# Kernel optimization log

Hardware: AMD Instinct MI355X
Metric: run time of the kernel (lower is better)

Reference implementation:

```python
import jax, jax.numpy as jnp
import numpy as np

NF = 24      # num_filters
KS = 5       # kernel_size
NB = 31      # num RBF basis
GAMMA = 0.1
EPS = 1e-3
B, H, W = 8, 180, 180


def setup_inputs() -> dict:
    key = jax.random.key(0)
    k1, k2, k3 = jax.random.split(key, 3)
    u = jax.random.uniform(k1, (B, 1, H, W), dtype=jnp.float32)
    f = jax.random.uniform(k2, (B, 1, H, W), dtype=jnp.float32)
    filters = jax.random.normal(k3, (NF, 1, KS, KS), dtype=jnp.float32) * 0.05
    mu = np.linspace(-1.0, 1.0, NB).astype(np.float32)
    x = np.linspace(-1.0, 1.0, 256).astype(np.float32)
    target = np.tanh(3.0 * x)
    basis = np.exp(-(x[:, None] - mu[None, :]) ** 2 / (2.0 * GAMMA ** 2))
    weights, _, _, _ = np.linalg.lstsq(basis, target, rcond=None)
    return {
        "u": u,
        "f": f,
        "filters": filters,
        "lambda_param": jnp.float32(0.1),
        "mu": jnp.asarray(mu),
        "weights": jnp.asarray(weights.astype(np.float32)),
    }


def reference(u, f, filters, lambda_param, mu, weights):
    dn = ("NCHW", "OIHW", "NCHW")
    pad = KS // 2
    # avg_pool2d(k=3, s=1, p=1) with count_include_pad=True (torch default): sum / 9
    u_sigma = jax.lax.reduce_window(
        u, 0.0, jax.lax.add,
        window_dimensions=(1, 1, 3, 3),
        window_strides=(1, 1, 1, 1),
        padding=[(0, 0), (0, 0), (1, 1), (1, 1)],
    ) / 9.0
    M = jnp.mean(u_sigma) + 0.001
    # all 24 per-filter convs as one grouped conv: [B,1,H,W] -> [B,NF,H,W]
    conv = jax.lax.conv_general_dilated(
        u, filters, (1, 1), [(pad, pad), (pad, pad)], dimension_numbers=dn
    )
    # RBF influence (identical frozen params for every filter)
    diff = conv[..., None] - mu                      # [B,NF,H,W,NB]
    phi = jnp.sum(weights * jnp.exp(-(diff ** 2) / (2.0 * GAMMA ** 2)), axis=-1)
    scaled_phi = (u_sigma / M) * phi                 # broadcast over NF channels
    # sum_i conv2d(scaled_phi_i, flip(k_i)) == one conv NF->1 with flipped kernels
    kT = jnp.flip(filters, axis=(2, 3)).transpose(1, 0, 2, 3)  # [1,NF,KS,KS]
    diffusion = jax.lax.conv_general_dilated(
        scaled_phi, kT, (1, 1), [(pad, pad), (pad, pad)], dimension_numbers=dn
    )
    reaction = lambda_param * (u - f) / (u * u + EPS)
    return jnp.clip(u - diffusion - reaction, 0.0, 1.0)
```

## Files before the change

### kernel.cpp

```cpp
#include <hip/hip_runtime.h>
#include <hip/hip_fp16.h>
#include <math.h>

#define HH 180
#define WW 180
#define BATCH 8
#define NF 24
#define NCP (NF / 2)
#define NB 31
#define HW (HH * WW)
#define NTOT (BATCH * HW)

#define TABN 1536
#define TAB_SCALE 512.0f
#define TAB_OFF 768.0f
#define L2E 1.4426950408889634f
#define RBF_L (-50.0f * L2E)

#if __has_builtin(__builtin_amdgcn_exp2f)
#define EXP2(x) __builtin_amdgcn_exp2f(x)
#else
#define EXP2(x) __expf((x) * 0.6931471805599453f)
#endif

typedef float v2f __attribute__((ext_vector_type(2)));

static __device__ __forceinline__ v2f splat2(float x) { v2f r; r.x = x; r.y = x; return r; }

__global__ __launch_bounds__(256) void k1_prepare(const float* __restrict__ u,
                                                  const float* __restrict__ wts,
                                                  const float* __restrict__ filters,
                                                  float* __restrict__ partials,
                                                  __half2* __restrict__ tab,
                                                  float* __restrict__ fT,
                                                  __half2* __restrict__ fTh) {
    __shared__ float sred[4];
    int blk = blockIdx.x, tid = threadIdx.x;
    if (blk < 128) {
        float v = 0.f;
        for (int i = blk * 256 + tid; i < NTOT / 4; i += 128 * 256) {
            float4 uv = ((const float4*)u)[i];
            int rem = (i * 4) % HW;
            int y = rem / WW, x0 = rem % WW;
            float cy = (y == 0 || y == HH - 1) ? 2.f : 3.f;
            float c0 = (x0 == 0) ? 2.f : 3.f;
            float c3 = (x0 + 3 == WW - 1) ? 2.f : 3.f;
            v += cy * (uv.x * c0 + (uv.y + uv.z) * 3.f + uv.w * c3);
        }
        #pragma unroll
        for (int off = 32; off; off >>= 1) v += __shfl_down(v, off, 64);
        int lane = tid & 63, wid = tid >> 6;
        if (lane == 0) sred[wid] = v;
        __syncthreads();
        if (tid == 0) partials[blk] = sred[0] + sred[1] + sred[2] + sred[3];
    } else if (blk < 134) {
        int e = (blk - 128) * 256 + tid;
        float w[NB];
        #pragma unroll
        for (int j = 0; j < NB; j++) w[j] = wts[j];
        float xa = -1.5f + (float)e * (1.f / TAB_SCALE);
        float xb = xa + (1.f / TAB_SCALE);
        float va = 0.f, vb = 0.f;
        #pragma unroll
        for (int j = 0; j < NB; j++) {
            float muj = -1.f + (float)j * (1.f / 15.f);
            float da = xa - muj, db = xb - muj;
            va = fmaf(w[j], EXP2(RBF_L * da * da), va);
            vb = fmaf(w[j], EXP2(RBF_L * db * db), vb);
        }
        tab[e] = __floats2half2_rn(va, vb - va);
    } else {
        for (int e = tid; e < NCP * 25; e += 256) {
            int cp = e / 25, k = e - cp * 25;
            float a = filters[(2 * cp) * 25 + k];
            float b = filters[(2 * cp + 1) * 25 + k];
            fT[2 * e] = a;
            fT[2 * e + 1] = b;
            fTh[e] = __floats2half2_rn(a, b);
        }
    }
}

#define TX 32
#define TY 12
#define TW 36
#define TH 16
#define TPTS (TW * TH)
#define UW 40
#define UH 20

static __device__ __forceinline__ float phi_lut(const __half2* stab, float c) {
    float tp = fmaf(c, TAB_SCALE, TAB_OFF);
    tp = fminf(fmaxf(tp, 0.f), (float)(TABN - 1));
    int i = (int)tp;
    float fr = tp - (float)i;
    float2 e = __half22float2(stab[i]);
    return fmaf(fr, e.y, e.x);
}

__global__ __launch_bounds__(256, 4) void k23_fused(const float* __restrict__ u,
                                                     const float* __restrict__ f,
                                                     const float* __restrict__ lam_p,
                                                     const float* __restrict__ partials,
                                                     const __half2* __restrict__ tab,
                                                     const v2f* __restrict__ fT2,
                                                     const __half2* __restrict__ fTh,
                                                     float* __restrict__ out) {
    __shared__ __align__(16) float su[UH * UW];
    __shared__ __align__(16) unsigned st[NCP * TPTS];
    __shared__ __align__(16) __half2 stab[TABN];
    __shared__ float sM[1];
    int b = blockIdx.z;
    int x0 = blockIdx.x * TX, y0 = blockIdx.y * TY;
    int tid = threadIdx.x;

    for (int e = tid; e < UH * UW; e += 256) {
        int r = e / UW, c = e - r * UW;
        int gy = y0 - 4 + r, gx = x0 - 4 + c;
        float v = 0.f;
        if (gy >= 0 && gy < HH && gx >= 0 && gx < WW) v = u[b * HW + gy * WW + gx];
        su[e] = v;
    }
    for (int e = tid; e < TABN / 4; e += 256)
        ((float4*)stab)[e] = ((const float4*)tab)[e];
    if (tid < 64) {
        float ps = partials[tid] + partials[tid + 64];
        #pragma unroll
        for (int off = 32; off; off >>= 1) ps += __shfl_down(ps, off, 64);
        if (tid == 0) sM[0] = 1.0f / (ps * (1.f / (9.f * (float)NTOT)) + 0.001f);
    }
    __syncthreads();

    if (tid < TPTS / 4) {
        int r = tid / (TW / 4), cq = (tid - r * (TW / 4)) * 4;
        float w[5][8];
        #pragma unroll
        for (int dy = 0; dy < 5; dy++) {
            float4 a = *(const float4*)&su[(r + dy) * UW + cq];
            float4 bb = *(const float4*)&su[(r + dy) * UW + cq + 4];
            w[dy][0] = a.x; w[dy][1] = a.y; w[dy][2] = a.z; w[dy][3] = a.w;
            w[dy][4] = bb.x; w[dy][5] = bb.y; w[dy][6] = bb.z; w[dy][7] = bb.w;
        }
        float S[6];
        #pragma unroll
        for (int m = 0; m < 6; m++) S[m] = w[1][m + 1] + w[2][m + 1] + w[3][m + 1];
        float us[4];
        int gy = y0 - 2 + r;
        bool okY = (gy >= 0 && gy < HH);
        #pragma unroll
        for (int p = 0; p < 4; p++) {
            us[p] = (S[p] + S[p + 1] + S[p + 2]) * (1.f / 9.f);
            int gx = x0 - 2 + cq + p;
            if (!(okY && gx >= 0 && gx < WW)) us[p] = 0.f;
        }
        #pragma unroll 2
        for (int cp = 0; cp < NCP; cp++) {
            v2f c2[4];
            #pragma unroll
            for (int p = 0; p < 4; p++) { c2[p].x = 0.f; c2[p].y = 0.f; }
            #pragma unroll
            for (int k = 0; k < 25; k++) {
                int dy = k / 5, dx = k - dy * 5;
                v2f fc = fT2[cp * 25 + k];
                #pragma unroll
                for (int p = 0; p < 4; p++)
                    c2[p] = __builtin_elementwise_fma(splat2(w[dy][dx + p]), fc, c2[p]);
            }
            uint4 pk;
            unsigned* pkp = (unsigned*)&pk;
            #pragma unroll
            for (int p = 0; p < 4; p++) {
                float vA = us[p] * phi_lut(stab, c2[p].x);
                float vB = us[p] * phi_lut(stab, c2[p].y);
                __half2 h = __floats2half2_rn(vA, vB);
                pkp[p] = *(unsigned*)&h;
            }
            *(uint4*)&st[cp * TPTS + r * TW + cq] = pk;
        }
    }
    __syncthreads();

    int txl = tid & 15, tyl = tid >> 4;
    int x = 2 * txl;
    if (tyl < TY) {
        float accf0 = 0.f, accf1 = 0.f;
        #pragma unroll 2
        for (int cp = 0; cp < NCP; cp++) {
            __half2 a0 = __floats2half2_rn(0.f, 0.f);
            __half2 a1 = a0;
            #pragma unroll
            for (int ey = 0; ey < 5; ey++) {
                int base = cp * TPTS + (tyl + 4 - ey) * TW + x;
                __half2 tc[6];
                #pragma unroll
                for (int j = 0; j < 6; j++) {
                    unsigned hv = st[base + j];
                    tc[j] = *(const __half2*)&hv;
                }
                #pragma unroll
                for (int ex = 0; ex < 5; ex++) {
                    __half2 fc = fTh[cp * 25 + ey * 5 + ex];
                    a0 = __hfma2(tc[4 - ex], fc, a0);
                    a1 = __hfma2(tc[5 - ex], fc, a1);
                }
            }
            float2 p0 = __half22float2(a0), p1 = __half22float2(a1);
            accf0 += p0.x + p0.y;
            accf1 += p1.x + p1.y;
        }
        int gx = x0 + x, gyy = y0 + tyl;
        if (gx < WW && gyy < HH) {
            float invM = sM[0];
            float lam = lam_p[0];
            int gidx = b * HW + gyy * WW + gx;
            float d0 = accf0 * invM;
            float d1 = accf1 * invM;
            float2 f2 = *(const float2*)&f[gidx];
            float u0 = su[(tyl + 4) * UW + (x + 4)];
            float u1 = su[(tyl + 4) * UW + (x + 5)];
            float2 o2;
            float val;
            val = u0 - d0 - lam * (u0 - f2.x) / (u0 * u0 + 1e-3f);
            o2.x = fminf(fmaxf(val, 0.f), 1.f);
            val = u1 - d1 - lam * (u1 - f2.y) / (u1 * u1 + 1e-3f);
            o2.y = fminf(fmaxf(val, 0.f), 1.f);
            *(float2*)&out[gidx] = o2;
        }
    }
}

extern "C" void kernel_launch(void* const* d_in, const int* in_sizes, int n_in,
                              void* d_out, int out_size, void* d_ws, size_t ws_size,
                              hipStream_t stream) {
    const float* u       = (const float*)d_in[0];
    const float* f       = (const float*)d_in[1];
    const float* filters = (const float*)d_in[2];
    const float* lam_p   = (const float*)d_in[3];
    const float* wts     = (const float*)d_in[5];
    float* out = (float*)d_out;

    float*   partials = (float*)d_ws;
    __half2* tab      = (__half2*)((char*)d_ws + 1024);
    float*   fT       = (float*)((char*)d_ws + 8192);
    __half2* fTh      = (__half2*)((char*)d_ws + 12288);

    k1_prepare<<<135, 256, 0, stream>>>(u, wts, filters, partials, tab, fT, fTh);

    dim3 g((WW + TX - 1) / TX, (HH + TY - 1) / TY, BATCH);
    k23_fused<<<g, 256, 0, stream>>>(u, f, lam_p, partials, tab, (const v2f*)fT, fTh, out);
}
```

Baseline: 88.54 us.

## Build RBF table per block, spread phase-one channels over all threads, vectorize LDS reads

The RBF lookup table is no longer built in the prepare kernel. Each fused block now computes an fp32 table of 1537 entries in shared memory. Phase one now uses all 256 threads instead of 144 by splitting the 12 channel pairs into four groups of three per quad, at the cost of each thread reloading its 5x8 stencil. The stage-two reads from shared memory are batched into uint2 loads. This trades redundant table computation in every block (31 exp per entry) for better thread utilization and removes the table round-trip through global memory.

Result: slower. 137.3 us (+55.1%).

```diff
diff --git a/kernel.cpp b/kernel.cpp
--- a/kernel.cpp
+++ b/kernel.cpp
@@ -11,7 +11,7 @@
 #define HW (HH * WW)
 #define NTOT (BATCH * HW)
 
-#define TABN 1536
+#define TABN 1537
 #define TAB_SCALE 512.0f
 #define TAB_OFF 768.0f
 #define L2E 1.4426950408889634f
@@ -28,10 +28,8 @@
 static __device__ __forceinline__ v2f splat2(float x) { v2f r; r.x = x; r.y = x; return r; }
 
 __global__ __launch_bounds__(256) void k1_prepare(const float* __restrict__ u,
-                                                  const float* __restrict__ wts,
                                                   const float* __restrict__ filters,
                                                   float* __restrict__ partials,
-                                                  __half2* __restrict__ tab,
                                                   float* __restrict__ fT,
                                                   __half2* __restrict__ fTh) {
     __shared__ float sred[4];
@@ -53,22 +51,6 @@
         if (lane == 0) sred[wid] = v;
         __syncthreads();
         if (tid == 0) partials[blk] = sred[0] + sred[1] + sred[2] + sred[3];
-    } else if (blk < 134) {
-        int e = (blk - 128) * 256 + tid;
-        float w[NB];
-        #pragma unroll
-        for (int j = 0; j < NB; j++) w[j] = wts[j];
-        float xa = -1.5f + (float)e * (1.f / TAB_SCALE);
-        float xb = xa + (1.f / TAB_SCALE);
-        float va = 0.f, vb = 0.f;
-        #pragma unroll
-        for (int j = 0; j < NB; j++) {
-            float muj = -1.f + (float)j * (1.f / 15.f);
-            float da = xa - muj, db = xb - muj;
-            va = fmaf(w[j], EXP2(RBF_L * da * da), va);
-            vb = fmaf(w[j], EXP2(RBF_L * db * db), vb);
-        }
-        tab[e] = __floats2half2_rn(va, vb - va);
     } else {
         for (int e = tid; e < NCP * 25; e += 256) {
             int cp = e / 25, k = e - cp * 25;
@@ -89,26 +71,17 @@
 #define UW 40
 #define UH 20
 
-static __device__ __forceinline__ float phi_lut(const __half2* stab, float c) {
-    float tp = fmaf(c, TAB_SCALE, TAB_OFF);
-    tp = fminf(fmaxf(tp, 0.f), (float)(TABN - 1));
-    int i = (int)tp;
-    float fr = tp - (float)i;
-    float2 e = __half22float2(stab[i]);
-    return fmaf(fr, e.y, e.x);
-}
-
 __global__ __launch_bounds__(256, 4) void k23_fused(const float* __restrict__ u,
                                                      const float* __restrict__ f,
                                                      const float* __restrict__ lam_p,
                                                      const float* __restrict__ partials,
-                                                     const __half2* __restrict__ tab,
+                                                     const float* __restrict__ wts,
                                                      const v2f* __restrict__ fT2,
                                                      const __half2* __restrict__ fTh,
                                                      float* __restrict__ out) {
     __shared__ __align__(16) float su[UH * UW];
     __shared__ __align__(16) unsigned st[NCP * TPTS];
-    __shared__ __align__(16) __half2 stab[TABN];
+    __shared__ __align__(16) float stab[TABN + 3];
     __shared__ float sM[1];
     int b = blockIdx.z;
     int x0 = blockIdx.x * TX, y0 = blockIdx.y * TY;
@@ -121,8 +94,22 @@
         if (gy >= 0 && gy < HH && gx >= 0 && gx < WW) v = u[b * HW + gy * WW + gx];
         su[e] = v;
     }
-    for (int e = tid; e < TABN / 4; e += 256)
-        ((float4*)stab)[e] = ((const float4*)tab)[e];
+    {
+        float w[NB];
+        #pragma unroll
+        for (int j = 0; j < NB; j++) w[j] = wts[j];
+        for (int e = tid; e < TABN; e += 256) {
+            float x = -1.5f + (float)e * (1.f / TAB_SCALE);
+            float va = 0.f;
+            #pragma unroll
+            for (int j = 0; j < NB; j++) {
+                float muj = -1.f + (float)j * (1.f / 15.f);
+                float d = x - muj;
+                va = fmaf(w[j], EXP2(RBF_L * d * d), va);
+            }
+            stab[e] = va;
+        }
+    }
     if (tid < 64) {
         float ps = partials[tid] + partials[tid + 64];
         #pragma unroll
@@ -131,8 +118,9 @@
     }
     __syncthreads();
 
-    if (tid < TPTS / 4) {
-        int r = tid / (TW / 4), cq = (tid - r * (TW / 4)) * 4;
+    for (int it = tid; it < 576; it += 256) {
+        int quad = it >> 2, grp = it & 3;
+        int r = quad / 9, cq = (quad - r * 9) * 4;
         float w[5][8];
         #pragma unroll
         for (int dy = 0; dy < 5; dy++) {
@@ -153,8 +141,9 @@
             int gx = x0 - 2 + cq + p;
             if (!(okY && gx >= 0 && gx < WW)) us[p] = 0.f;
         }
-        #pragma unroll 2
-        for (int cp = 0; cp < NCP; cp++) {
+        #pragma unroll
+        for (int j3 = 0; j3 < 3; j3++) {
+            int cp = grp * 3 + j3;
             v2f c2[4];
             #pragma unroll
             for (int p = 0; p < 4; p++) { c2[p].x = 0.f; c2[p].y = 0.f; }
@@ -170,8 +159,16 @@
             unsigned* pkp = (unsigned*)&pk;
             #pragma unroll
             for (int p = 0; p < 4; p++) {
-                float vA = us[p] * phi_lut(stab, c2[p].x);
-                float vB = us[p] * phi_lut(stab, c2[p].y);
+                float tpA = fmaf(c2[p].x, TAB_SCALE, TAB_OFF);
+                tpA = fminf(fmaxf(tpA, 0.f), (float)(TABN - 2));
+                int iA = (int)tpA; float frA = tpA - (float)iA;
+                float a0 = stab[iA], a1 = stab[iA + 1];
+                float vA = us[p] * fmaf(frA, a1 - a0, a0);
+                float tpB = fmaf(c2[p].y, TAB_SCALE, TAB_OFF);
+                tpB = fminf(fmaxf(tpB, 0.f), (float)(TABN - 2));
+                int iB = (int)tpB; float frB = tpB - (float)iB;
+                float b0 = stab[iB], b1 = stab[iB + 1];
+                float vB = us[p] * fmaf(frB, b1 - b0, b0);
                 __half2 h = __floats2half2_rn(vA, vB);
                 pkp[p] = *(unsigned*)&h;
             }
@@ -186,15 +183,22 @@
         float accf0 = 0.f, accf1 = 0.f;
         #pragma unroll 2
         for (int cp = 0; cp < NCP; cp++) {
+            uint2 ld[5][3];
+            #pragma unroll
+            for (int ey = 0; ey < 5; ey++) {
+                int base = cp * TPTS + (tyl + 4 - ey) * TW + x;
+                ld[ey][0] = *(const uint2*)&st[base];
+                ld[ey][1] = *(const uint2*)&st[base + 2];
+                ld[ey][2] = *(const uint2*)&st[base + 4];
+            }
             __half2 a0 = __floats2half2_rn(0.f, 0.f);
             __half2 a1 = a0;
             #pragma unroll
             for (int ey = 0; ey < 5; ey++) {
-                int base = cp * TPTS + (tyl + 4 - ey) * TW + x;
                 __half2 tc[6];
                 #pragma unroll
                 for (int j = 0; j < 6; j++) {
-                    unsigned hv = st[base + j];
+                    unsigned hv = (j & 1) ? ld[ey][j >> 1].y : ld[ey][j >> 1].x;
                     tc[j] = *(const __half2*)&hv;
                 }
                 #pragma unroll
@@ -240,12 +244,11 @@
     float* out = (float*)d_out;
 
     float*   partials = (float*)d_ws;
-    __half2* tab      = (__half2*)((char*)d_ws + 1024);
-    float*   fT       = (float*)((char*)d_ws + 8192);
-    __half2* fTh      = (__half2*)((char*)d_ws + 12288);
-
-    k1_prepare<<<135, 256, 0, stream>>>(u, wts, filters, partials, tab, fT, fTh);
+    float*   fT       = (float*)((char*)d_ws + 1024);
+    __half2* fTh      = (__half2*)((char*)d_ws + 4096);
+
+    k1_prepare<<<129, 256, 0, stream>>>(u, filters, partials, fT, fTh);
 
     dim3 g((WW + TX - 1) / TX, (HH + TY - 1) / TY, BATCH);
-    k23_fused<<<g, 256, 0, stream>>>(u, f, lam_p, partials, tab, (const v2f*)fT, fTh, out);
+    k23_fused<<<g, 256, 0, stream>>>(u, f, lam_p, partials, wts, (const v2f*)fT, fTh, out);
 }
```
